# Optimization experiments

Hardware: AMD Instinct MI355X
Metric: run time of the kernel (lower is better)

## Reference

```python
import jax, jax.numpy as jnp
import numpy as np

N_NODES = 50000
N_EDGES = 800000
IN_CH = 128
HID_CH = 128
OUT_CH = 64
K = 25
LRELU_SLOPE = 0.01  # torch.nn.LeakyReLU default
NORM_EPS = 1e-12    # F.normalize default eps


def setup_inputs() -> dict:
    key = jax.random.key(0)
    ks = jax.random.split(key, 8)
    x = jax.random.normal(ks[0], (N_NODES, IN_CH), dtype=jnp.float32)
    edge_index = jax.random.randint(ks[1], (2, N_EDGES), 0, N_NODES, dtype=jnp.int32)
    # ChebConv per-order weights [K, in, hid] + bias
    W = jax.random.normal(ks[2], (K, IN_CH, HID_CH), dtype=jnp.float32) / np.sqrt(IN_CH)
    b = jax.random.normal(ks[3], (HID_CH,), dtype=jnp.float32) * 0.01
    # mu / logstd linear heads
    w_mu = jax.random.normal(ks[4], (HID_CH, OUT_CH), dtype=jnp.float32) / np.sqrt(HID_CH)
    b_mu = jax.random.normal(ks[5], (OUT_CH,), dtype=jnp.float32) * 0.01
    w_ls = jax.random.normal(ks[6], (HID_CH, OUT_CH), dtype=jnp.float32) / np.sqrt(HID_CH)
    b_ls = jax.random.normal(ks[7], (OUT_CH,), dtype=jnp.float32) * 0.01
    return {"x": x, "edge_index": edge_index, "W": W, "b": b,
            "w_mu": w_mu, "b_mu": b_mu, "w_ls": w_ls, "b_ls": b_ls}


def _cheb_conv(x, edge_index, W, b):
    # PyG ChebConv with normalization='sym', lambda_max=2.0:
    # scaled Laplacian L~ = L - I = -D^{-1/2} A D^{-1/2} (diagonal nets to zero)
    src, dst = edge_index[0], edge_index[1]
    deg = jax.ops.segment_sum(jnp.ones(src.shape[0], x.dtype), src, num_segments=x.shape[0])
    dis = jnp.where(deg > 0, jax.lax.rsqrt(jnp.where(deg > 0, deg, 1.0)), 0.0)
    enorm = -dis[src] * dis[dst]  # [E]

    def prop(h):  # out[i] = sum_{(j->i)} enorm_e * h[j]
        return jax.ops.segment_sum(enorm[:, None] * h[src], dst, num_segments=h.shape[0])

    tx0 = x
    tx1 = prop(x)
    out0 = tx0 @ W[0] + tx1 @ W[1]

    def step(carry, Wk):
        t1, t0, acc = carry
        t2 = 2.0 * prop(t1) - t0  # Chebyshev recurrence
        return (t2, t1, acc + t2 @ Wk), None

    (_, _, out), _ = jax.lax.scan(step, (tx1, tx0, out0), W[2:])
    return out + b


def reference(x, edge_index, W, b, w_mu, b_mu, w_ls, b_ls):
    h = _cheb_conv(x, edge_index, W, b)
    # eval mode: dropout is identity
    h = jnp.where(h > 0, h, LRELU_SLOPE * h)
    mu = h @ w_mu + b_mu
    ls = h @ w_ls + b_ls
    nrm = jnp.sqrt(jnp.sum(ls * ls, axis=1, keepdims=True))
    logstd = ls / jnp.maximum(nrm, NORM_EPS) * 1.8
    zeta = mu  # eval-mode reparam returns mu
    return (mu, logstd, zeta)
```

## Files before the change

kernel.cpp:

```cpp
#include <hip/hip_runtime.h>
#include <hip/hip_fp16.h>

#define N_NODES 50000
#define N_EDGES 800000
#define CH 128
#define OUT_CH 64
#define K_ORD 25
#define SLICE ((size_t)N_NODES * CH)

typedef __attribute__((ext_vector_type(8))) short s16x8;
typedef __attribute__((ext_vector_type(4))) float f32x4;

union U4H8 { uint4 u; __half2 h2[4]; ushort us[8]; };

__global__ void count_kernel(const int* __restrict__ ei, int* __restrict__ deg_i,
                             int* __restrict__ indeg, int E) {
    int e = blockIdx.x * blockDim.x + threadIdx.x;
    if (e >= E) return;
    int s = ei[e];
    int d = ei[E + e];
    atomicAdd(&deg_i[s], 1);
    atomicAdd(&indeg[d], 1);
}

__global__ __launch_bounds__(256) void scan1_kernel(const int* __restrict__ indeg,
                                                    int* __restrict__ loc,
                                                    int* __restrict__ bsum, int n) {
    __shared__ int tmp[256];
    int tid = threadIdx.x;
    int i = blockIdx.x * 256 + tid;
    int v = (i < n) ? indeg[i] : 0;
    tmp[tid] = v;
    __syncthreads();
    for (int off = 1; off < 256; off <<= 1) {
        int t = (tid >= off) ? tmp[tid - off] : 0;
        __syncthreads();
        tmp[tid] += t;
        __syncthreads();
    }
    if (i < n) loc[i] = tmp[tid] - v;
    if (tid == 255) bsum[blockIdx.x] = tmp[255];
}

__global__ __launch_bounds__(256) void scan2_kernel(int* __restrict__ bsum, int nb) {
    __shared__ int tmp[256];
    int tid = threadIdx.x;
    int v = (tid < nb) ? bsum[tid] : 0;
    tmp[tid] = v;
    __syncthreads();
    for (int off = 1; off < 256; off <<= 1) {
        int t = (tid >= off) ? tmp[tid - off] : 0;
        __syncthreads();
        tmp[tid] += t;
        __syncthreads();
    }
    if (tid < nb) bsum[tid] = tmp[tid] - v;
    if (tid == 255) bsum[nb] = tmp[255];
}

__global__ __launch_bounds__(256) void scan3_kernel(const int* __restrict__ loc,
                                                    const int* __restrict__ bsum,
                                                    int* __restrict__ rowptr,
                                                    int* __restrict__ cursor, int n, int nb) {
    int i = blockIdx.x * 256 + threadIdx.x;
    if (i < n) {
        int r = loc[i] + bsum[i >> 8];
        rowptr[i] = r;
        cursor[i] = r;
    }
    if (i == n) rowptr[n] = bsum[nb];
}

__global__ void scatter_kernel(const int* __restrict__ ei, int* __restrict__ cursor,
                               int* __restrict__ col, int E) {
    int e = blockIdx.x * blockDim.x + threadIdx.x;
    if (e >= E) return;
    int s = ei[e];
    int d = ei[E + e];
    int pos = atomicAdd(&cursor[d], 1);
    col[pos] = s;
}

__global__ __launch_bounds__(256) void scaleprep_kernel(const int* __restrict__ deg_i,
                                                        float* __restrict__ beta,
                                                        float* __restrict__ alpha,
                                                        float* __restrict__ gam, int n) {
    int i = blockIdx.x * 256 + threadIdx.x;
    if (i >= n) return;
    int dg = deg_i[i];
    if (dg > 0) {
        float fd = (float)dg;
        beta[i] = -2.f / fd;
        alpha[i] = rsqrtf(fd);
        gam[i] = sqrtf(fd);
    } else {
        beta[i] = 0.f;
        alpha[i] = 1.f;
        gam[i] = 1.f;
    }
}

__global__ __launch_bounds__(256) void cvt_kernel(const float* __restrict__ in,
                                                  const float* __restrict__ alpha,
                                                  ushort* __restrict__ out, int n8) {
    int i = blockIdx.x * 256 + threadIdx.x;
    if (i >= n8) return;
    int row = i >> 4;
    float al = alpha[row];
    float4 a = ((const float4*)in)[2 * i];
    float4 b = ((const float4*)in)[2 * i + 1];
    U4H8 p;
    p.h2[0] = __float22half2_rn(make_float2(al * a.x, al * a.y));
    p.h2[1] = __float22half2_rn(make_float2(al * a.z, al * a.w));
    p.h2[2] = __float22half2_rn(make_float2(al * b.x, al * b.y));
    p.h2[3] = __float22half2_rn(make_float2(al * b.z, al * b.w));
    ((uint4*)out)[i] = p.u;
}

__global__ __launch_bounds__(256) void wprep_kernel(const float* __restrict__ W,
                                                    ushort* __restrict__ WT) {
    int idx = blockIdx.x * 256 + threadIdx.x;
    if (idx >= K_ORD * 128 * 32) return;
    int c4 = idx & 31;
    int nrow = (idx >> 5) & 127;
    int k = idx >> 12;
    const float* Wk = W + (size_t)k * CH * CH;
    ushort o[4];
    #pragma unroll
    for (int j = 0; j < 4; ++j)
        o[j] = __half_as_ushort(__float2half_rn(Wk[(c4 * 4 + j) * CH + nrow]));
    *(ushort2*)(WT + (size_t)k * CH * CH + nrow * CH + c4 * 4)     = make_ushort2(o[0], o[1]);
    *(ushort2*)(WT + (size_t)k * CH * CH + nrow * CH + c4 * 4 + 2) = make_ushort2(o[2], o[3]);
}

__global__ __launch_bounds__(256) void prop_kernel(
    const ushort* __restrict__ tin, const ushort* __restrict__ tprev,
    ushort* __restrict__ tout, const int* __restrict__ rowptr,
    const int* __restrict__ col, const float* __restrict__ beta, int n, int mode) {
    int wid = blockIdx.x * 4 + (threadIdx.x >> 6);
    if (wid >= n) return;
    int lane = threadIdx.x & 63;
    int g = lane >> 4, sub = lane & 15;
    int beg = rowptr[wid], end = rowptr[wid + 1];
    float acc[8] = {0.f, 0.f, 0.f, 0.f, 0.f, 0.f, 0.f, 0.f};
    for (int e0 = beg; e0 < end; e0 += 64) {
        int ne = min(64, end - e0);
        int c = 0;
        if (lane < ne) c = col[e0 + lane];
        for (int j16 = 0; j16 < ne; j16 += 16) {
            U4H8 v[4];
            float m[4];
            #pragma unroll
            for (int u = 0; u < 4; ++u) {
                int j = j16 + u * 4 + g;
                int cj = __shfl(c, j & 63);
                m[u] = (j < ne) ? 1.f : 0.f;
                v[u].u = ((const uint4*)(tin + (size_t)cj * CH))[sub];
            }
            #pragma unroll
            for (int u = 0; u < 4; ++u) {
                #pragma unroll
                for (int t = 0; t < 4; ++t) {
                    float2 f = __half22float2(v[u].h2[t]);
                    acc[2 * t]     = fmaf(m[u], f.x, acc[2 * t]);
                    acc[2 * t + 1] = fmaf(m[u], f.y, acc[2 * t + 1]);
                }
            }
        }
    }
    #pragma unroll
    for (int i = 0; i < 8; ++i) {
        acc[i] += __shfl_xor(acc[i], 16);
        acc[i] += __shfl_xor(acc[i], 32);
    }
    if (g == 0) {
        float bt = beta[wid];
        size_t base = (size_t)wid * CH + sub * 8;
        float r[8];
        if (mode) {
            U4H8 pv;
            pv.u = *(const uint4*)(tprev + base);
            #pragma unroll
            for (int t = 0; t < 4; ++t) {
                float2 f = __half22float2(pv.h2[t]);
                r[2 * t]     = fmaf(bt, acc[2 * t],     -f.x);
                r[2 * t + 1] = fmaf(bt, acc[2 * t + 1], -f.y);
            }
        } else {
            float hb = 0.5f * bt;
            #pragma unroll
            for (int i = 0; i < 8; ++i) r[i] = hb * acc[i];
        }
        U4H8 p;
        p.h2[0] = __float22half2_rn(make_float2(r[0], r[1]));
        p.h2[1] = __float22half2_rn(make_float2(r[2], r[3]));
        p.h2[2] = __float22half2_rn(make_float2(r[4], r[5]));
        p.h2[3] = __float22half2_rn(make_float2(r[6], r[7]));
        *(uint4*)(tout + base) = p.u;
    }
}

__global__ __launch_bounds__(256) void gemm_kernel(
    const ushort* __restrict__ T, size_t kstride, const ushort* __restrict__ WT,
    const float* __restrict__ gam, float* __restrict__ C,
    int M, int wk0, int nk, int betaf) {
    __shared__ ushort As[128 * 128];
    __shared__ ushort Ws[128 * 128];
    int tid = threadIdx.x;
    int row0 = blockIdx.x * 128;
    int wave = tid >> 6, lane = tid & 63;
    int wrow = wave * 32;
    int lr = lane & 15, kg = lane >> 4;

    f32x4 acc[2][8];
    #pragma unroll
    for (int a = 0; a < 2; ++a)
        #pragma unroll
        for (int c = 0; c < 8; ++c)
            acc[a][c] = (f32x4){0.f, 0.f, 0.f, 0.f};

    for (int ks = 0; ks < nk; ++ks) {
        const ushort* Ak = T + (size_t)ks * kstride;
        const ushort* Wk = WT + (size_t)(wk0 + ks) * (CH * CH);
        #pragma unroll
        for (int i = 0; i < 8; ++i) {
            int idx = tid + i * 256;
            int r = idx >> 4, gg = idx & 15;
            int gr = row0 + r;
            U4H8 hv;
            hv.u = make_uint4(0u, 0u, 0u, 0u);
            if (gr < M) {
                hv.u = ((const uint4*)(Ak + (size_t)gr * CH))[gg];
                float gm = gam[gr];
                #pragma unroll
                for (int t = 0; t < 4; ++t) {
                    float2 f = __half22float2(hv.h2[t]);
                    hv.h2[t] = __float22half2_rn(make_float2(gm * f.x, gm * f.y));
                }
            }
            int gs = gg ^ (r & 15);
            *(uint4*)(&As[r * 128 + gs * 8]) = hv.u;
        }
        #pragma unroll
        for (int i = 0; i < 8; ++i) {
            int idx = tid + i * 256;
            int r = idx >> 4, gg = idx & 15;
            uint4 v = ((const uint4*)(Wk + (size_t)r * CH))[gg];
            int gs = gg ^ (r & 15);
            *(uint4*)(&Ws[r * 128 + gs * 8]) = v;
        }
        __syncthreads();

        #pragma unroll
        for (int kc = 0; kc < 4; ++kc) {
            int gbase = kc * 4 + kg;
            int gs = gbase ^ lr;
            s16x8 a0 = *(const s16x8*)(&As[(wrow + lr) * 128 + gs * 8]);
            s16x8 a1 = *(const s16x8*)(&As[(wrow + 16 + lr) * 128 + gs * 8]);
            #pragma unroll
            for (int c = 0; c < 8; ++c) {
                s16x8 bfr = *(const s16x8*)(&Ws[(c * 16 + lr) * 128 + gs * 8]);
                acc[0][c] = __builtin_amdgcn_mfma_f32_16x16x32_f16(a0, bfr, acc[0][c], 0, 0, 0);
                acc[1][c] = __builtin_amdgcn_mfma_f32_16x16x32_f16(a1, bfr, acc[1][c], 0, 0, 0);
            }
        }
        __syncthreads();
    }

    #pragma unroll
    for (int rf = 0; rf < 2; ++rf)
        #pragma unroll
        for (int c = 0; c < 8; ++c)
            #pragma unroll
            for (int j = 0; j < 4; ++j) {
                int gr = row0 + wrow + rf * 16 + kg * 4 + j;
                int gc = c * 16 + lr;
                if (gr < M) {
                    float v = acc[rf][c][j];
                    if (betaf) v += C[(size_t)gr * 128 + gc];
                    C[(size_t)gr * 128 + gc] = v;
                }
            }
}

__global__ __launch_bounds__(256) void head_kernel(
    const float* __restrict__ acc_in, const float* __restrict__ b,
    const float* __restrict__ w_mu, const float* __restrict__ b_mu,
    const float* __restrict__ w_ls, const float* __restrict__ b_ls,
    float* __restrict__ out, int M) {
    __shared__ ushort Hs[128 * 128];
    __shared__ ushort Ws[128 * 128];
    __shared__ float s_b[128];
    int tid = threadIdx.x;
    int row0 = blockIdx.x * 128;
    if (tid < 128) s_b[tid] = b[tid];
    __syncthreads();

    #pragma unroll
    for (int i = 0; i < 16; ++i) {
        int idx = tid + i * 256;
        int r = idx >> 5, c4 = idx & 31;
        float4 v = make_float4(0.f, 0.f, 0.f, 0.f);
        int gr = row0 + r;
        if (gr < M) v = ((const float4*)(acc_in + (size_t)gr * CH))[c4];
        float hv[4] = { v.x, v.y, v.z, v.w };
        #pragma unroll
        for (int j = 0; j < 4; ++j) {
            float h = hv[j] + s_b[c4 * 4 + j];
            hv[j] = h > 0.f ? h : 0.01f * h;
        }
        __half2 p0 = __float22half2_rn(make_float2(hv[0], hv[1]));
        __half2 p1 = __float22half2_rn(make_float2(hv[2], hv[3]));
        int gg = c4 >> 1, hh = c4 & 1;
        int gs = gg ^ (r & 15);
        uint2 pk;
        pk.x = *(unsigned int*)&p0;
        pk.y = *(unsigned int*)&p1;
        *(uint2*)(&Hs[r * 128 + gs * 8 + hh * 4]) = pk;
    }
    #pragma unroll
    for (int i = 0; i < 16; ++i) {
        int idx = tid + i * 256;
        int k = idx >> 5, n4 = idx & 31;
        const float* src = (n4 < 16) ? w_mu : w_ls;
        float4 v = ((const float4*)src)[k * 16 + (n4 & 15)];
        int gk = k >> 3, kk = k & 7;
        float vv[4] = { v.x, v.y, v.z, v.w };
        #pragma unroll
        for (int j = 0; j < 4; ++j) {
            int nn = n4 * 4 + j;
            int gs = gk ^ (nn & 15);
            Ws[nn * 128 + gs * 8 + kk] = __half_as_ushort(__float2half_rn(vv[j]));
        }
    }
    __syncthreads();

    int wave = tid >> 6, lane = tid & 63;
    int wrow = wave * 32;
    int lr = lane & 15, kg = lane >> 4;
    f32x4 acc[2][8];
    #pragma unroll
    for (int a = 0; a < 2; ++a)
        #pragma unroll
        for (int c = 0; c < 8; ++c)
            acc[a][c] = (f32x4){0.f, 0.f, 0.f, 0.f};

    #pragma unroll
    for (int kc = 0; kc < 4; ++kc) {
        int gbase = kc * 4 + kg;
        int gs = gbase ^ lr;
        s16x8 a0 = *(const s16x8*)(&Hs[(wrow + lr) * 128 + gs * 8]);
        s16x8 a1 = *(const s16x8*)(&Hs[(wrow + 16 + lr) * 128 + gs * 8]);
        #pragma unroll
        for (int c = 0; c < 8; ++c) {
            s16x8 bfr = *(const s16x8*)(&Ws[(c * 16 + lr) * 128 + gs * 8]);
            acc[0][c] = __builtin_amdgcn_mfma_f32_16x16x32_f16(a0, bfr, acc[0][c], 0, 0, 0);
            acc[1][c] = __builtin_amdgcn_mfma_f32_16x16x32_f16(a1, bfr, acc[1][c], 0, 0, 0);
        }
    }

    #pragma unroll
    for (int rf = 0; rf < 2; ++rf)
        #pragma unroll
        for (int j = 0; j < 4; ++j) {
            int gr = row0 + wrow + rf * 16 + kg * 4 + j;
            float muv[4], lsv[4];
            float s2 = 0.f;
            #pragma unroll
            for (int c = 0; c < 4; ++c) {
                muv[c] = acc[rf][c][j] + b_mu[c * 16 + lr];
                float l = acc[rf][4 + c][j] + b_ls[c * 16 + lr];
                lsv[c] = l;
                s2 = fmaf(l, l, s2);
            }
            s2 += __shfl_xor(s2, 1);
            s2 += __shfl_xor(s2, 2);
            s2 += __shfl_xor(s2, 4);
            s2 += __shfl_xor(s2, 8);
            float sc = 1.8f / fmaxf(sqrtf(s2), 1e-12f);
            if (gr < M) {
                size_t base = (size_t)gr * OUT_CH;
                #pragma unroll
                for (int c = 0; c < 4; ++c) {
                    int gc = c * 16 + lr;
                    out[base + gc] = muv[c];
                    out[(size_t)N_NODES * OUT_CH + base + gc] = lsv[c] * sc;
                    out[2 * (size_t)N_NODES * OUT_CH + base + gc] = muv[c];
                }
            }
        }
}

extern "C" void kernel_launch(void* const* d_in, const int* in_sizes, int n_in,
                              void* d_out, int out_size, void* d_ws, size_t ws_size,
                              hipStream_t stream) {
    const float* x    = (const float*)d_in[0];
    const int*   ei   = (const int*)d_in[1];
    const float* W    = (const float*)d_in[2];
    const float* b    = (const float*)d_in[3];
    const float* w_mu = (const float*)d_in[4];
    const float* b_mu = (const float*)d_in[5];
    const float* w_ls = (const float*)d_in[6];
    const float* b_ls = (const float*)d_in[7];

    const int N = N_NODES, E = N_EDGES;
    const int NB = (N + 255) / 256;
    char* p = (char*)d_ws;
    auto alloc = [&](size_t bytes) {
        char* r = p;
        p += (bytes + 511) & ~(size_t)511;
        return r;
    };
    int*    deg_i  = (int*)alloc((size_t)N * 4);
    int*    indeg  = (int*)alloc((size_t)N * 4);
    int*    rowptr = (int*)alloc((size_t)(N + 1) * 4);
    int*    cursor = (int*)alloc((size_t)N * 4);
    int*    loc    = (int*)alloc((size_t)N * 4);
    int*    bsum   = (int*)alloc((size_t)(NB + 1) * 4);
    int*    col    = (int*)alloc((size_t)E * 4);
    float*  beta   = (float*)alloc((size_t)N * 4);
    float*  alpha  = (float*)alloc((size_t)N * 4);
    float*  gam    = (float*)alloc((size_t)N * 4);
    ushort* WT     = (ushort*)alloc((size_t)K_ORD * CH * CH * 2);
    float*  accbuf = (float*)alloc((size_t)N * CH * 4);

    size_t used = (size_t)(p - (char*)d_ws);
    bool bigpath = ws_size >= used + (size_t)K_ORD * SLICE * 2 + (1u << 20);

    (void)hipMemsetAsync(deg_i, 0, (size_t)N * 4, stream);
    (void)hipMemsetAsync(indeg, 0, (size_t)N * 4, stream);

    count_kernel<<<(E + 255) / 256, 256, 0, stream>>>(ei, deg_i, indeg, E);
    scan1_kernel<<<NB, 256, 0, stream>>>(indeg, loc, bsum, N);
    scan2_kernel<<<1, 256, 0, stream>>>(bsum, NB);
    scan3_kernel<<<NB, 256, 0, stream>>>(loc, bsum, rowptr, cursor, N, NB);
    scatter_kernel<<<(E + 255) / 256, 256, 0, stream>>>(ei, cursor, col, E);
    scaleprep_kernel<<<(N + 255) / 256, 256, 0, stream>>>(deg_i, beta, alpha, gam, N);
    wprep_kernel<<<(K_ORD * 128 * 32 + 255) / 256, 256, 0, stream>>>(W, WT);

    int gemm_grid = (N + 127) / 128;
    int prop_grid = (N + 3) / 4;
    int cvt_grid = (N * 16 + 255) / 256;

    if (bigpath) {
        ushort* T = (ushort*)alloc((size_t)K_ORD * SLICE * 2);
        cvt_kernel<<<cvt_grid, 256, 0, stream>>>(x, alpha, T, N * 16);
        prop_kernel<<<prop_grid, 256, 0, stream>>>(T, T, T + SLICE,
                                                   rowptr, col, beta, N, 0);
        for (int k = 2; k < K_ORD; ++k)
            prop_kernel<<<prop_grid, 256, 0, stream>>>(
                T + (size_t)(k - 1) * SLICE, T + (size_t)(k - 2) * SLICE,
                T + (size_t)k * SLICE, rowptr, col, beta, N, 1);
        gemm_kernel<<<gemm_grid, 256, 0, stream>>>(T, SLICE, WT, gam, accbuf,
                                                   N, 0, K_ORD, 0);
    } else {
        ushort* r0 = (ushort*)alloc(SLICE * 2);
        ushort* r1 = (ushort*)alloc(SLICE * 2);
        ushort* r2 = (ushort*)alloc(SLICE * 2);
        ushort* Ss[3] = { r0, r1, r2 };
        cvt_kernel<<<cvt_grid, 256, 0, stream>>>(x, alpha, r0, N * 16);
        gemm_kernel<<<gemm_grid, 256, 0, stream>>>(r0, 0, WT, gam, accbuf, N, 0, 1, 0);
        prop_kernel<<<prop_grid, 256, 0, stream>>>(r0, r0, r1, rowptr, col, beta, N, 0);
        gemm_kernel<<<gemm_grid, 256, 0, stream>>>(r1, 0, WT, gam, accbuf, N, 1, 1, 1);
        for (int k = 2; k < K_ORD; ++k) {
            prop_kernel<<<prop_grid, 256, 0, stream>>>(
                Ss[(k - 1) % 3], Ss[(k - 2) % 3], Ss[k % 3], rowptr, col, beta, N, 1);
            gemm_kernel<<<gemm_grid, 256, 0, stream>>>(Ss[k % 3], 0, WT, gam, accbuf,
                                                       N, k, 1, 1);
        }
    }

    head_kernel<<<gemm_grid, 256, 0, stream>>>(accbuf, b, w_mu, b_mu, w_ls, b_ls,
                                               (float*)d_out, N);
}
```

Baseline: 1.516 ms.

## Privatize degree atomics into copies and split final GEMM over K in two halves

Degree counting and CSR scatter now use eight private copies of the counter arrays, selected by block index, which reduces atomic contention on hot nodes. Fold and cursor-init kernels merge the copies, and each copy's cursor starts at its own offset within the row. The big-path GEMM over all 25 Chebyshev orders is split along the order dimension across two grid slices writing separate accumulators, which doubles block count for better CU occupancy. The head kernel then sums the two accumulators, at the cost of extra memory for the second accumulator and more small kernel launches.

```diff
diff --git a/kernel.cpp b/kernel.cpp
--- a/kernel.cpp
+++ b/kernel.cpp
@@ -7,20 +7,32 @@
 #define OUT_CH 64
 #define K_ORD 25
 #define SLICE ((size_t)N_NODES * CH)
+#define NCOPY 8
 
 typedef __attribute__((ext_vector_type(8))) short s16x8;
 typedef __attribute__((ext_vector_type(4))) float f32x4;
 
 union U4H8 { uint4 u; __half2 h2[4]; ushort us[8]; };
 
-__global__ void count_kernel(const int* __restrict__ ei, int* __restrict__ deg_i,
-                             int* __restrict__ indeg, int E) {
+__global__ void count_kernel(const int* __restrict__ ei, int* __restrict__ deg8,
+                             int* __restrict__ indeg8, int E, int n) {
     int e = blockIdx.x * blockDim.x + threadIdx.x;
     if (e >= E) return;
+    int cp = blockIdx.x & (NCOPY - 1);
     int s = ei[e];
     int d = ei[E + e];
-    atomicAdd(&deg_i[s], 1);
-    atomicAdd(&indeg[d], 1);
+    atomicAdd(&deg8[cp * n + s], 1);
+    atomicAdd(&indeg8[cp * n + d], 1);
+}
+
+__global__ __launch_bounds__(256) void fold_kernel(const int* __restrict__ indeg8,
+                                                   int* __restrict__ indegN, int n) {
+    int i = blockIdx.x * 256 + threadIdx.x;
+    if (i >= n) return;
+    int s = 0;
+    #pragma unroll
+    for (int c = 0; c < NCOPY; ++c) s += indeg8[c * n + i];
+    indegN[i] = s;
 }
 
 __global__ __launch_bounds__(256) void scan1_kernel(const int* __restrict__ indeg,
@@ -60,34 +72,45 @@
 
 __global__ __launch_bounds__(256) void scan3_kernel(const int* __restrict__ loc,
                                                     const int* __restrict__ bsum,
-                                                    int* __restrict__ rowptr,
-                                                    int* __restrict__ cursor, int n, int nb) {
+                                                    int* __restrict__ rowptr, int n, int nb) {
     int i = blockIdx.x * 256 + threadIdx.x;
-    if (i < n) {
-        int r = loc[i] + bsum[i >> 8];
-        rowptr[i] = r;
-        cursor[i] = r;
-    }
+    if (i < n) rowptr[i] = loc[i] + bsum[i >> 8];
     if (i == n) rowptr[n] = bsum[nb];
 }
 
-__global__ void scatter_kernel(const int* __restrict__ ei, int* __restrict__ cursor,
-                               int* __restrict__ col, int E) {
+__global__ __launch_bounds__(256) void cursorinit_kernel(const int* __restrict__ rowptr,
+                                                         const int* __restrict__ indeg8,
+                                                         int* __restrict__ cursor8, int n) {
+    int i = blockIdx.x * 256 + threadIdx.x;
+    if (i >= n) return;
+    int base = rowptr[i];
+    #pragma unroll
+    for (int c = 0; c < NCOPY; ++c) {
+        cursor8[c * n + i] = base;
+        base += indeg8[c * n + i];
+    }
+}
+
+__global__ void scatter_kernel(const int* __restrict__ ei, int* __restrict__ cursor8,
+                               int* __restrict__ col, int E, int n) {
     int e = blockIdx.x * blockDim.x + threadIdx.x;
     if (e >= E) return;
+    int cp = blockIdx.x & (NCOPY - 1);
     int s = ei[e];
     int d = ei[E + e];
-    int pos = atomicAdd(&cursor[d], 1);
+    int pos = atomicAdd(&cursor8[cp * n + d], 1);
     col[pos] = s;
 }
 
-__global__ __launch_bounds__(256) void scaleprep_kernel(const int* __restrict__ deg_i,
+__global__ __launch_bounds__(256) void scaleprep_kernel(const int* __restrict__ deg8,
                                                         float* __restrict__ beta,
                                                         float* __restrict__ alpha,
                                                         float* __restrict__ gam, int n) {
     int i = blockIdx.x * 256 + threadIdx.x;
     if (i >= n) return;
-    int dg = deg_i[i];
+    int dg = 0;
+    #pragma unroll
+    for (int c = 0; c < NCOPY; ++c) dg += deg8[c * n + i];
     if (dg > 0) {
         float fd = (float)dg;
         beta[i] = -2.f / fd;
@@ -202,8 +225,11 @@
 
 __global__ __launch_bounds__(256) void gemm_kernel(
     const ushort* __restrict__ T, size_t kstride, const ushort* __restrict__ WT,
-    const float* __restrict__ gam, float* __restrict__ C,
-    int M, int wk0, int nk, int betaf) {
+    const float* __restrict__ gam, float* __restrict__ C0, float* __restrict__ C1,
+    int M, int k0a, int nka, int k0b, int nkb, int betaf) {
+    int wk0 = (blockIdx.y == 0) ? k0a : k0b;
+    int nk  = (blockIdx.y == 0) ? nka : nkb;
+    float* C = (blockIdx.y == 0) ? C0 : C1;
     __shared__ ushort As[128 * 128];
     __shared__ ushort Ws[128 * 128];
     int tid = threadIdx.x;
@@ -220,7 +246,7 @@
             acc[a][c] = (f32x4){0.f, 0.f, 0.f, 0.f};
 
     for (int ks = 0; ks < nk; ++ks) {
-        const ushort* Ak = T + (size_t)ks * kstride;
+        const ushort* Ak = T + (size_t)(wk0 + ks) * kstride;
         const ushort* Wk = WT + (size_t)(wk0 + ks) * (CH * CH);
         #pragma unroll
         for (int i = 0; i < 8; ++i) {
@@ -284,10 +310,10 @@
 }
 
 __global__ __launch_bounds__(256) void head_kernel(
-    const float* __restrict__ acc_in, const float* __restrict__ b,
-    const float* __restrict__ w_mu, const float* __restrict__ b_mu,
-    const float* __restrict__ w_ls, const float* __restrict__ b_ls,
-    float* __restrict__ out, int M) {
+    const float* __restrict__ acc0, const float* __restrict__ acc1, int use2,
+    const float* __restrict__ b, const float* __restrict__ w_mu,
+    const float* __restrict__ b_mu, const float* __restrict__ w_ls,
+    const float* __restrict__ b_ls, float* __restrict__ out, int M) {
     __shared__ ushort Hs[128 * 128];
     __shared__ ushort Ws[128 * 128];
     __shared__ float s_b[128];
@@ -302,7 +328,13 @@
         int r = idx >> 5, c4 = idx & 31;
         float4 v = make_float4(0.f, 0.f, 0.f, 0.f);
         int gr = row0 + r;
-        if (gr < M) v = ((const float4*)(acc_in + (size_t)gr * CH))[c4];
+        if (gr < M) {
+            v = ((const float4*)(acc0 + (size_t)gr * CH))[c4];
+            if (use2) {
+                float4 w = ((const float4*)(acc1 + (size_t)gr * CH))[c4];
+                v.x += w.x; v.y += w.y; v.z += w.z; v.w += w.w;
+            }
+        }
         float hv[4] = { v.x, v.y, v.z, v.w };
         #pragma unroll
         for (int j = 0; j < 4; ++j) {
@@ -411,31 +443,35 @@
         p += (bytes + 511) & ~(size_t)511;
         return r;
     };
-    int*    deg_i  = (int*)alloc((size_t)N * 4);
-    int*    indeg  = (int*)alloc((size_t)N * 4);
-    int*    rowptr = (int*)alloc((size_t)(N + 1) * 4);
-    int*    cursor = (int*)alloc((size_t)N * 4);
-    int*    loc    = (int*)alloc((size_t)N * 4);
-    int*    bsum   = (int*)alloc((size_t)(NB + 1) * 4);
-    int*    col    = (int*)alloc((size_t)E * 4);
-    float*  beta   = (float*)alloc((size_t)N * 4);
-    float*  alpha  = (float*)alloc((size_t)N * 4);
-    float*  gam    = (float*)alloc((size_t)N * 4);
-    ushort* WT     = (ushort*)alloc((size_t)K_ORD * CH * CH * 2);
-    float*  accbuf = (float*)alloc((size_t)N * CH * 4);
+    int*    deg8    = (int*)alloc((size_t)NCOPY * N * 4);
+    int*    indeg8  = (int*)alloc((size_t)NCOPY * N * 4);
+    int*    cursor8 = (int*)alloc((size_t)NCOPY * N * 4);
+    int*    indegN  = (int*)alloc((size_t)N * 4);
+    int*    rowptr  = (int*)alloc((size_t)(N + 1) * 4);
+    int*    loc     = (int*)alloc((size_t)N * 4);
+    int*    bsum    = (int*)alloc((size_t)(NB + 1) * 4);
+    int*    col     = (int*)alloc((size_t)E * 4);
+    float*  beta    = (float*)alloc((size_t)N * 4);
+    float*  alpha   = (float*)alloc((size_t)N * 4);
+    float*  gam     = (float*)alloc((size_t)N * 4);
+    ushort* WT      = (ushort*)alloc((size_t)K_ORD * CH * CH * 2);
+    float*  accbuf0 = (float*)alloc((size_t)N * CH * 4);
+    float*  accbuf1 = (float*)alloc((size_t)N * CH * 4);
 
     size_t used = (size_t)(p - (char*)d_ws);
     bool bigpath = ws_size >= used + (size_t)K_ORD * SLICE * 2 + (1u << 20);
 
-    (void)hipMemsetAsync(deg_i, 0, (size_t)N * 4, stream);
-    (void)hipMemsetAsync(indeg, 0, (size_t)N * 4, stream);
-
-    count_kernel<<<(E + 255) / 256, 256, 0, stream>>>(ei, deg_i, indeg, E);
-    scan1_kernel<<<NB, 256, 0, stream>>>(indeg, loc, bsum, N);
+    (void)hipMemsetAsync(deg8, 0, (size_t)NCOPY * N * 4, stream);
+    (void)hipMemsetAsync(indeg8, 0, (size_t)NCOPY * N * 4, stream);
+
+    count_kernel<<<(E + 255) / 256, 256, 0, stream>>>(ei, deg8, indeg8, E, N);
+    fold_kernel<<<NB, 256, 0, stream>>>(indeg8, indegN, N);
+    scan1_kernel<<<NB, 256, 0, stream>>>(indegN, loc, bsum, N);
     scan2_kernel<<<1, 256, 0, stream>>>(bsum, NB);
-    scan3_kernel<<<NB, 256, 0, stream>>>(loc, bsum, rowptr, cursor, N, NB);
-    scatter_kernel<<<(E + 255) / 256, 256, 0, stream>>>(ei, cursor, col, E);
-    scaleprep_kernel<<<(N + 255) / 256, 256, 0, stream>>>(deg_i, beta, alpha, gam, N);
+    scan3_kernel<<<NB + 1, 256, 0, stream>>>(loc, bsum, rowptr, N, NB);
+    cursorinit_kernel<<<NB, 256, 0, stream>>>(rowptr, indeg8, cursor8, N);
+    scatter_kernel<<<(E + 255) / 256, 256, 0, stream>>>(ei, cursor8, col, E, N);
+    scaleprep_kernel<<<NB, 256, 0, stream>>>(deg8, beta, alpha, gam, N);
     wprep_kernel<<<(K_ORD * 128 * 32 + 255) / 256, 256, 0, stream>>>(W, WT);
 
     int gemm_grid = (N + 127) / 128;
@@ -451,25 +487,31 @@
             prop_kernel<<<prop_grid, 256, 0, stream>>>(
                 T + (size_t)(k - 1) * SLICE, T + (size_t)(k - 2) * SLICE,
                 T + (size_t)k * SLICE, rowptr, col, beta, N, 1);
-        gemm_kernel<<<gemm_grid, 256, 0, stream>>>(T, SLICE, WT, gam, accbuf,
-                                                   N, 0, K_ORD, 0);
+        gemm_kernel<<<dim3(gemm_grid, 2), 256, 0, stream>>>(
+            T, SLICE, WT, gam, accbuf0, accbuf1, N, 0, 13, 13, 12, 0);
+        head_kernel<<<gemm_grid, 256, 0, stream>>>(accbuf0, accbuf1, 1, b,
+                                                   w_mu, b_mu, w_ls, b_ls,
+                                                   (float*)d_out, N);
     } else {
         ushort* r0 = (ushort*)alloc(SLICE * 2);
         ushort* r1 = (ushort*)alloc(SLICE * 2);
         ushort* r2 = (ushort*)alloc(SLICE * 2);
         ushort* Ss[3] = { r0, r1, r2 };
         cvt_kernel<<<cvt_grid, 256, 0, stream>>>(x, alpha, r0, N * 16);
-        gemm_kernel<<<gemm_grid, 256, 0, stream>>>(r0, 0, WT, gam, accbuf, N, 0, 1, 0);
+        gemm_kernel<<<dim3(gemm_grid, 1), 256, 0, stream>>>(
+            r0, 0, WT, gam, accbuf0, accbuf0, N, 0, 1, 0, 0, 0);
         prop_kernel<<<prop_grid, 256, 0, stream>>>(r0, r0, r1, rowptr, col, beta, N, 0);
-        gemm_kernel<<<gemm_grid, 256, 0, stream>>>(r1, 0, WT, gam, accbuf, N, 1, 1, 1);
+        gemm_kernel<<<dim3(gemm_grid, 1), 256, 0, stream>>>(
+            r1, 0, WT + (size_t)CH * CH, gam, accbuf0, accbuf0, N, 0, 1, 0, 0, 1);
         for (int k = 2; k < K_ORD; ++k) {
             prop_kernel<<<prop_grid, 256, 0, stream>>>(
                 Ss[(k - 1) % 3], Ss[(k - 2) % 3], Ss[k % 3], rowptr, col, beta, N, 1);
-            gemm_kernel<<<gemm_grid, 256, 0, stream>>>(Ss[k % 3], 0, WT, gam, accbuf,
-                                                       N, k, 1, 1);
-        }
-    }
-
-    head_kernel<<<gemm_grid, 256, 0, stream>>>(accbuf, b, w_mu, b_mu, w_ls, b_ls,
-                                               (float*)d_out, N);
-}
+            gemm_kernel<<<dim3(gemm_grid, 1), 256, 0, stream>>>(
+                Ss[k % 3], 0, WT + (size_t)k * CH * CH, gam, accbuf0, accbuf0,
+                N, 0, 1, 0, 0, 1);
+        }
+        head_kernel<<<gemm_grid, 256, 0, stream>>>(accbuf0, accbuf0, 0, b,
+                                                   w_mu, b_mu, w_ls, b_ls,
+                                                   (float*)d_out, N);
+    }
+}
```

New measurement: 1.506 ms. Within noise of the previous version (-0.6%).
